# Performance work log

Measured on AMD Instinct MI355X. Metric: run time of the kernel, lower is better.

## Reference

```python
import jax, jax.numpy as jnp
import numpy as np

B, S, D, H, F, E, K = 2, 2048, 1024, 16, 4096, 8, 2
EPS = 1e-6


def setup_inputs() -> dict:
    key = jax.random.key(0)
    ks = jax.random.split(key, 9)
    s = 0.02
    return {
        "x": jax.random.normal(ks[0], (B, S, D), jnp.float32),
        "n1_w": jnp.ones((D,), jnp.float32),
        "n2_w": jnp.ones((D,), jnp.float32),
        "wq": jax.random.normal(ks[1], (D, D), jnp.float32) * s,
        "wk": jax.random.normal(ks[2], (D, D), jnp.float32) * s,
        "wv": jax.random.normal(ks[3], (D, D), jnp.float32) * s,
        "wo": jax.random.normal(ks[4], (D, D), jnp.float32) * s,
        "router_w": jax.random.normal(ks[5], (E, D), jnp.float32) * s,  # nn.Linear(D, E, bias=False)
        "w1": jax.random.normal(ks[6], (E, D, F), jnp.float32) * s,
        "b1": jnp.zeros((E, F), jnp.float32),
        "w2": jax.random.normal(ks[7], (E, F, D), jnp.float32) * s,
        "b2": jnp.zeros((E, D), jnp.float32),
    }


def _rms(t, w):
    return t * w * jax.lax.rsqrt(jnp.mean(t * t, axis=-1, keepdims=True) + EPS)


def reference(x, n1_w, n2_w, wq, wk, wv, wo, router_w, w1, b1, w2, b2):
    hd = D // H
    # --- pre-norm causal multi-head self-attention ---
    h = _rms(x, n1_w)
    q = (h @ wq).reshape(B, S, H, hd)
    k = (h @ wk).reshape(B, S, H, hd)
    v = (h @ wv).reshape(B, S, H, hd)
    scores = jnp.einsum("bqhd,bkhd->bhqk", q, k) * (hd ** -0.5)
    causal = jnp.tril(jnp.ones((S, S), bool))
    scores = jnp.where(causal, scores, jnp.float32(-1e9))
    attn = jax.nn.softmax(scores, axis=-1)
    attn_out = jnp.einsum("bhqk,bkhd->bqhd", attn, v).reshape(B, S, D) @ wo
    x = x + attn_out
    # --- pre-norm MoE MLP: dense experts + top-k weighted combine ---
    h2 = _rms(x, n2_w)
    logits = h2 @ router_w.T                         # [B,S,E]
    probs = jax.nn.softmax(logits, axis=-1)
    topv, topi = jax.lax.top_k(probs, K)             # [B,S,K]
    topv = topv / jnp.sum(topv, axis=-1, keepdims=True)  # renormalized top-k gates
    bi = jnp.arange(B)[:, None, None]
    si = jnp.arange(S)[None, :, None]
    gates = jnp.zeros_like(probs).at[bi, si, topi].set(topv)  # sparse gates [B,S,E]
    eh = jax.nn.gelu(jnp.einsum("bsd,edf->ebsf", h2, w1) + b1[:, None, None, :])
    eo = jnp.einsum("ebsf,efd->ebsd", eh, w2) + b2[:, None, None, :]
    y = jnp.einsum("ebsd,bse->bsd", eo, gates)
    return x + y
```

## Files before the change

### kernel.cpp

```cpp
#include <hip/hip_runtime.h>
#include <hip/hip_bf16.h>


typedef float fx4 __attribute__((ext_vector_type(4)));
typedef short sx4 __attribute__((ext_vector_type(4)));
typedef short sx8 __attribute__((ext_vector_type(8)));
typedef int ix2 __attribute__((ext_vector_type(2)));
typedef int ix4 __attribute__((ext_vector_type(4)));

#define DEVFN static __device__ __forceinline__
#define MFMA16(a, b, c) __builtin_amdgcn_mfma_f32_16x16x32_bf16((a), (b), (c), 0, 0, 0)

typedef __attribute__((address_space(1))) const void GASV;
typedef __attribute__((address_space(3))) void LASV;

DEVFN short f2bf(float f) {
  unsigned u = __float_as_uint(f);
  return (short)((u + 0x7FFFu + ((u >> 16) & 1u)) >> 16);
}
DEVFN float bf2f(short s) { return __uint_as_float(((unsigned)(unsigned short)s) << 16); }

DEVFN int cvt_pk_bf16(float a, float b) {
  int r;
  asm("v_cvt_pk_bf16_f32 %0, %1, %2" : "=v"(r) : "v"(a), "v"(b));
  return r;
}

DEVFN void gll16(const short* g, short* l) {
  __builtin_amdgcn_global_load_lds((GASV*)g, (LASV*)l, 16, 0, 0);
}

template <int BK>
DEVFN int swzr(int row) {
  if constexpr (BK == 64)
    return row & 7;
  else
    return (row ^ (row >> 2)) & 3;
}

DEVFN float fast_gelu(float x) {
  float u = 0.7978845608028654f * (x + 0.044715f * x * x * x);
  float e = __expf(2.0f * u);
  float t = 1.0f - 2.0f / (1.0f + e);
  return 0.5f * x * (1.0f + t);
}

DEVFN float wsum64(float v) {
#pragma unroll
  for (int m = 1; m < 64; m <<= 1) v += __shfl_xor(v, m);
  return v;
}

template <int SPLIT>
__global__ __launch_bounds__(256) void transpose_k(const float* in, short* oh, short* ol,
                                                   int R, int C) {
  __shared__ float t[64][65];
  const int c0 = blockIdx.x * 64, r0 = blockIdx.y * 64;
  const long long bofs = (long long)blockIdx.z * R * C;
  in += bofs;
  oh += bofs;
  if (SPLIT) ol += bofs;
  const int tid = threadIdx.x;
  const int rr = tid >> 4, cc4 = (tid & 15) * 4;
#pragma unroll
  for (int i = 0; i < 4; ++i) {
    int r = i * 16 + rr;
    fx4 v = *(const fx4*)(in + (long long)(r0 + r) * C + c0 + cc4);
    t[r][cc4] = v.x;
    t[r][cc4 + 1] = v.y;
    t[r][cc4 + 2] = v.z;
    t[r][cc4 + 3] = v.w;
  }
  __syncthreads();
#pragma unroll
  for (int i = 0; i < 4; ++i) {
    int oc = i * 16 + rr;
    sx4 hv, lv;
#pragma unroll
    for (int j = 0; j < 4; ++j) {
      float v = t[cc4 + j][oc];
      short hi = f2bf(v);
      hv[j] = hi;
      if (SPLIT) lv[j] = f2bf(v - bf2f(hi));
    }
    *(sx4*)(oh + (long long)(c0 + oc) * R + r0 + cc4) = hv;
    if (SPLIT) *(sx4*)(ol + (long long)(c0 + oc) * R + r0 + cc4) = lv;
  }
}

template <int SPLIT>
__global__ __launch_bounds__(256) void rms_k(const float* x, const float* w, short* hh,
                                             short* hl) {
  const int row = blockIdx.x, tid = threadIdx.x;
  const fx4 v = ((const fx4*)(x + (long long)row * 1024))[tid];
  float ss = v.x * v.x + v.y * v.y + v.z * v.z + v.w * v.w;
  ss = wsum64(ss);
  __shared__ float red[4];
  if ((tid & 63) == 0) red[tid >> 6] = ss;
  __syncthreads();
  ss = red[0] + red[1] + red[2] + red[3];
  const float rr = rsqrtf(ss * (1.0f / 1024.0f) + 1e-6f);
  const fx4 wv = ((const fx4*)w)[tid];
  float vals[4] = {v.x * wv.x * rr, v.y * wv.y * rr, v.z * wv.z * rr, v.w * wv.w * rr};
  sx4 oh, ol;
#pragma unroll
  for (int c = 0; c < 4; ++c) {
    short hi = f2bf(vals[c]);
    oh[c] = hi;
    if (SPLIT) ol[c] = f2bf(vals[c] - bf2f(hi));
  }
  ((sx4*)(hh + (long long)row * 1024))[tid] = oh;
  if (SPLIT) ((sx4*)(hl + (long long)row * 1024))[tid] = ol;
}

struct GemmArgs {
  const short *Ah, *Al, *Bh, *Bl;
  int K, lda, ldb, ldc;
  long long strideBe;
  short *out_h, *out_l;
  float* out_f;
  const float* bias;
  const int* tile_info;
  const float* row_gate;
  const int* row_token;
};

template <int TERMS, int BM, int BK, int BN, int EPI, int PIPE, int NTHR, int WCN>
__global__ __launch_bounds__(NTHR) void gemm_k(GemmArgs a) {
  const int tid = threadIdx.x, lane = tid & 63, wave = tid >> 6;
  const int gx = gridDim.x;
  const int nwg = gx * (int)gridDim.y;
  int flat = (int)blockIdx.y * gx + (int)blockIdx.x;
  flat = (flat & 7) * (nwg >> 3) + (flat >> 3);
  const int bx = flat % gx;
  const int by = flat / gx;

  int row0, expert = 0, valid = BM;
  if constexpr (EPI == 3 || EPI == 5) {
    const int* ti = a.tile_info + by * 4;
    expert = ti[0];
    row0 = ti[1];
    valid = ti[2];
    if (valid == 0) return;
  } else {
    row0 = by * BM;
  }
  const short* Ap = a.Ah;
  const short* Bp = a.Bh + ((EPI == 3 || EPI == 5) ? (long long)expert * a.strideBe : 0ll);
  const int kbeg = blockIdx.z * a.K;

  constexpr int CH = BK / 8;
  constexpr int NIA = (BM * CH) / NTHR;
  constexpr int NIB = (BN * CH) / NTHR;
  constexpr int ASZ = BM * BK;
  constexpr int BSZ = BN * BK;
  constexpr int WRN = (NTHR / 64) / WCN;
  constexpr int MI = BM / WRN / 16;
  constexpr int TN = BN / WCN / 16;
  constexpr int NB = PIPE ? 2 : 1;

  __shared__ short Ash[NB][ASZ];
  __shared__ short Bsh[NB][BSZ];
  __shared__ short Asl[TERMS == 3 ? NB : 1][TERMS == 3 ? ASZ : 1];
  __shared__ short Bsl[TERMS == 3 ? NB : 1][TERMS == 3 ? BSZ : 1];

  fx4 acc[MI][TN] = {};
  const int wr = wave / WCN, wc = wave % WCN;

  long long aoff[NIA];
#pragma unroll
  for (int i = 0; i < NIA; ++i) {
    int row = (i * NTHR + tid) / CH;
    if constexpr (EPI == 3)
      aoff[i] = (long long)a.row_token[row0 + row] * a.lda;
    else
      aoff[i] = (long long)(row0 + row) * a.lda;
  }

  auto stage = [&](int s, int k0) {
#pragma unroll
    for (int i = 0; i < NIA; ++i) {
      int t = i * NTHR + tid;
      int row = t / CH, c = t % CH;
      int cc = c ^ swzr<BK>(row);
      int lbase = (i * NTHR + wave * 64) * 8;
      long long acol = kbeg + k0 + cc * 8;
      gll16(Ap + aoff[i] + acol, &Ash[s][lbase]);
      if constexpr (TERMS == 3)
        gll16(a.Al + aoff[i] + acol, &Asl[s][lbase]);
    }
#pragma unroll
    for (int i = 0; i < NIB; ++i) {
      int t = i * NTHR + tid;
      int row = t / CH, c = t % CH;
      int cc = c ^ swzr<BK>(row);
      int lbase = (i * NTHR + wave * 64) * 8;
      long long acol = kbeg + k0 + cc * 8;
      gll16(Bp + (long long)(bx * BN + row) * a.ldb + acol, &Bsh[s][lbase]);
      if constexpr (TERMS == 3)
        gll16(a.Bl + (long long)(bx * BN + row) * a.ldb + acol, &Bsl[s][lbase]);
    }
  };

  auto compute = [&](int s) {
#pragma unroll
    for (int kk = 0; kk < BK / 32; ++kk) {
      sx8 ah[MI], bh[TN], al_[MI], bl_[TN];
#pragma unroll
      for (int mi = 0; mi < MI; ++mi) {
        int row = wr * (BM / WRN) + mi * 16 + (lane & 15);
        int sc = (kk * 4 + (lane >> 4)) ^ swzr<BK>(row);
        ah[mi] = *(const sx8*)&Ash[s][row * BK + sc * 8];
        if constexpr (TERMS == 3) al_[mi] = *(const sx8*)&Asl[s][row * BK + sc * 8];
      }
#pragma unroll
      for (int ni = 0; ni < TN; ++ni) {
        int row = wc * (BN / WCN) + ni * 16 + (lane & 15);
        int sc = (kk * 4 + (lane >> 4)) ^ swzr<BK>(row);
        bh[ni] = *(const sx8*)&Bsh[s][row * BK + sc * 8];
        if constexpr (TERMS == 3) bl_[ni] = *(const sx8*)&Bsl[s][row * BK + sc * 8];
      }
#pragma unroll
      for (int mi = 0; mi < MI; ++mi)
#pragma unroll
        for (int ni = 0; ni < TN; ++ni) {
          acc[mi][ni] = MFMA16(ah[mi], bh[ni], acc[mi][ni]);
          if constexpr (TERMS == 3) {
            acc[mi][ni] = MFMA16(ah[mi], bl_[ni], acc[mi][ni]);
            acc[mi][ni] = MFMA16(al_[mi], bh[ni], acc[mi][ni]);
          }
        }
    }
  };

  const int NT = a.K / BK;
  stage(0, 0);
  __syncthreads();
  for (int t = 0; t < NT; ++t) {
    if constexpr (PIPE) {
      if (t + 1 < NT) stage((t + 1) & 1, (t + 1) * BK);
      compute(t & 1);
      if (t + 1 < NT) __syncthreads();
    } else {
      compute(0);
      if (t + 1 < NT) {
        __syncthreads();
        stage(0, (t + 1) * BK);
        __syncthreads();
      }
    }
  }

#pragma unroll
  for (int mi = 0; mi < MI; ++mi)
#pragma unroll
    for (int ni = 0; ni < TN; ++ni) {
      fx4 v = acc[mi][ni];
      int rl = wr * (BM / WRN) + mi * 16 + ((lane >> 4) << 2);
      int col = bx * BN + wc * (BN / WCN) + ni * 16 + (lane & 15);
#pragma unroll
      for (int j = 0; j < 4; ++j) {
        int r = rl + j;
        long long grow = (long long)row0 + r;
        float xv = v[j];
        if constexpr (EPI == 1) {
          short hi = f2bf(xv);
          a.out_h[grow * a.ldc + col] = hi;
          a.out_l[grow * a.ldc + col] = f2bf(xv - bf2f(hi));
        } else if constexpr (EPI == 3) {
          xv += a.bias[expert * a.ldc + col];
          a.out_h[grow * a.ldc + col] = f2bf(fast_gelu(xv));
        } else if constexpr (EPI == 5) {
          if (r < valid) {
            xv += a.bias[expert * a.ldc + col];
            float g = a.row_gate[grow];
            a.out_h[grow * a.ldc + col] = f2bf(xv * g);
          }
        } else if constexpr (EPI == 6) {
          a.out_f[(long long)blockIdx.z * 4194304 + grow * a.ldc + col] = xv;
        }
      }
    }
}

__global__ __launch_bounds__(256) void combine_rms_router_k(
    const float* p0, const float* p1, const float* resid, const float* w,
    const float* rw, float* out, short* h2, int* tok_e, float* tok_g) {
  const int row = blockIdx.x, tid = threadIdx.x;
  const long long base = (long long)row * 1024 + tid * 4;
  fx4 a = *(const fx4*)(p0 + base);
  fx4 b = *(const fx4*)(p1 + base);
  fx4 r = *(const fx4*)(resid + base);
  fx4 o;
  float ss = 0.f;
#pragma unroll
  for (int j = 0; j < 4; ++j) {
    o[j] = a[j] + b[j] + r[j];
    ss += o[j] * o[j];
  }
  *(fx4*)(out + base) = o;
  ss = wsum64(ss);
  __shared__ float red[4];
  if ((tid & 63) == 0) red[tid >> 6] = ss;
  __syncthreads();
  ss = red[0] + red[1] + red[2] + red[3];
  const float rr = rsqrtf(ss * (1.0f / 1024.0f) + 1e-6f);
  const fx4 wv = ((const fx4*)w)[tid];
  fx4 t;
#pragma unroll
  for (int j = 0; j < 4; ++j) t[j] = o[j] * wv[j];
  sx4 oh;
#pragma unroll
  for (int c = 0; c < 4; ++c) oh[c] = f2bf(t[c] * rr);
  ((sx4*)(h2 + (long long)row * 1024))[tid] = oh;

  float lg[8];
#pragma unroll
  for (int e = 0; e < 8; ++e) {
    fx4 rv = ((const fx4*)(rw + e * 1024))[tid];
    float acc = t[0] * rv[0] + t[1] * rv[1] + t[2] * rv[2] + t[3] * rv[3];
    lg[e] = wsum64(acc);
  }
  __shared__ float lred[8][4];
  if ((tid & 63) == 0) {
#pragma unroll
    for (int e = 0; e < 8; ++e) lred[e][tid >> 6] = lg[e];
  }
  __syncthreads();
  if (tid == 0) {
    float logit[8];
#pragma unroll
    for (int e = 0; e < 8; ++e)
      logit[e] = (lred[e][0] + lred[e][1] + lred[e][2] + lred[e][3]) * rr;
    float mx = logit[0];
#pragma unroll
    for (int e = 1; e < 8; ++e) mx = fmaxf(mx, logit[e]);
    float pe[8];
#pragma unroll
    for (int e = 0; e < 8; ++e) pe[e] = expf(logit[e] - mx);
    int e1 = 0;
    float b1v = pe[0];
#pragma unroll
    for (int e = 1; e < 8; ++e)
      if (pe[e] > b1v) {
        b1v = pe[e];
        e1 = e;
      }
    int e2 = -1;
    float b2v = -1.0f;
#pragma unroll
    for (int e = 0; e < 8; ++e)
      if (e != e1 && pe[e] > b2v) {
        b2v = pe[e];
        e2 = e;
      }
    float inv = 1.0f / (b1v + b2v);
    tok_e[(long long)row * 2] = e1;
    tok_e[(long long)row * 2 + 1] = e2;
    tok_g[(long long)row * 2] = b1v * inv;
    tok_g[(long long)row * 2 + 1] = b2v * inv;
  }
}

__global__ __launch_bounds__(256) void combine_k(const int* row_of_entry,
                                                 const short* eo, float* out) {
  const int tid = threadIdx.x, lane = tid & 63, wave = tid >> 6;
  const long long token = (long long)blockIdx.x * 4 + wave;
  const int r1 = row_of_entry[token * 2];
  const int r2 = row_of_entry[token * 2 + 1];
  const sx8* e1 = (const sx8*)(eo + (long long)r1 * 1024);
  const sx8* e2 = (const sx8*)(eo + (long long)r2 * 1024);
  float* op = out + token * 1024;
#pragma unroll
  for (int half = 0; half < 2; ++half) {
    sx8 va = e1[lane + half * 64];
    sx8 vb = e2[lane + half * 64];
    int cb = (lane + half * 64) * 8;
#pragma unroll
    for (int q = 0; q < 2; ++q) {
      fx4 o = *(const fx4*)(op + cb + q * 4);
#pragma unroll
      for (int j = 0; j < 4; ++j) o[j] += bf2f(va[q * 4 + j]) + bf2f(vb[q * 4 + j]);
      *(fx4*)(op + cb + q * 4) = o;
    }
  }
}

__global__ __launch_bounds__(128, 2) void flash_k(const short* __restrict__ qkv_h,
                                                  const short* __restrict__ qkv_l,
                                                  short* __restrict__ ao_h,
                                                  short* __restrict__ ao_l) {
  const int tid = threadIdx.x, lane = tid & 63, wave = tid >> 6;
  const int l15 = lane & 15, g = lane >> 4;
  const int qt = (blockIdx.x + blockIdx.y) & 31;
  const int bh = blockIdx.y;
  const int b = bh >> 4, h = bh & 15;
  const long long base = (long long)b * 2048 * 3072;
  const int qw = qt * 64 + wave * 32;

  __shared__ short Kh[4096], Kl[4096];
  __shared__ int VTh[64 * 34], VTl[64 * 34];

  sx8 qh[2][2], ql[2][2];
#pragma unroll
  for (int mb = 0; mb < 2; ++mb)
#pragma unroll
    for (int kk = 0; kk < 2; ++kk) {
      long long qofs =
          base + (long long)(qw + mb * 16 + l15) * 3072 + h * 64 + kk * 32 + g * 8;
      qh[mb][kk] = *(const sx8*)(qkv_h + qofs);
      ql[mb][kk] = *(const sx8*)(qkv_l + qofs);
    }

  fx4 o[2][4] = {};
  float m_r[2] = {-3e38f, -3e38f}, l_r[2] = {0.f, 0.f};

  const int krow0 = tid >> 3;
  const int kc8 = (tid & 7) * 8;
  const int kswz = ((tid & 7) ^ (krow0 & 7)) * 8;
  const int vu = tid >> 3;
  const int vd0 = (tid & 7) * 8;

  sx8 kr[4], krl[4], vr[4], vrl[4];

  auto load_tile = [&](int kt2) {
    const long long tb = base + (long long)(kt2 * 64) * 3072 + h * 64;
#pragma unroll
    for (int s = 0; s < 4; ++s) {
      long long gofs = tb + 1024 + (long long)(s * 16 + krow0) * 3072 + kc8;
      kr[s] = *(const sx8*)(qkv_h + gofs);
      krl[s] = *(const sx8*)(qkv_l + gofs);
    }
#pragma unroll
    for (int k4 = 0; k4 < 4; ++k4) {
      long long gofs = tb + 2048 + (long long)(4 * vu + k4) * 3072 + vd0;
      vr[k4] = *(const sx8*)(qkv_h + gofs);
      vrl[k4] = *(const sx8*)(qkv_l + gofs);
    }
  };

  const int nt = qt + 1;
  load_tile(0);

  for (int kt = 0; kt < nt; ++kt) {
#pragma unroll
    for (int s = 0; s < 4; ++s) {
      *(sx8*)&Kh[(s * 16 + krow0) * 64 + kswz] = kr[s];
      *(sx8*)&Kl[(s * 16 + krow0) * 64 + kswz] = krl[s];
    }
#pragma unroll
    for (int i = 0; i < 8; ++i) {
      int d = vd0 + i;
      ix2 wh, wl;
      wh[0] = (int)(unsigned short)vr[0][i] | ((int)(unsigned short)vr[1][i] << 16);
      wh[1] = (int)(unsigned short)vr[2][i] | ((int)(unsigned short)vr[3][i] << 16);
      wl[0] = (int)(unsigned short)vrl[0][i] | ((int)(unsigned short)vrl[1][i] << 16);
      wl[1] = (int)(unsigned short)vrl[2][i] | ((int)(unsigned short)vrl[3][i] << 16);
      *(ix2*)&VTh[d * 34 + 2 * vu] = wh;
      *(ix2*)&VTl[d * 34 + 2 * vu] = wl;
    }
    __syncthreads();

    if (kt + 1 < nt) load_tile(kt + 1);

    const bool diag = (kt == nt - 1);
    float pvv[2][16];
#pragma unroll
    for (int kc = 0; kc < 4; ++kc) {
      int row = kc * 16 + l15;
      int rsw = row & 7;
      fx4 s0 = {}, s1 = {};
#pragma unroll
      for (int kk = 0; kk < 2; ++kk) {
        int sc = ((kk * 4 + g) ^ rsw) * 8;
        sx8 khf = *(const sx8*)&Kh[row * 64 + sc];
        sx8 klf = *(const sx8*)&Kl[row * 64 + sc];
        s0 = MFMA16(khf, qh[0][kk], s0);
        s1 = MFMA16(khf, qh[1][kk], s1);
        s0 = MFMA16(khf, ql[0][kk], s0);
        s1 = MFMA16(khf, ql[1][kk], s1);
        s0 = MFMA16(klf, qh[0][kk], s0);
        s1 = MFMA16(klf, qh[1][kk], s1);
      }
#pragma unroll
      for (int j = 0; j < 4; ++j) {
        pvv[0][kc * 4 + j] = s0[j];
        pvv[1][kc * 4 + j] = s1[j];
      }
    }

    sx8 pah[2][2], pal[2][2];
#pragma unroll
    for (int mb = 0; mb < 2; ++mb) {
      const int qidx = qw + mb * 16 + l15;
      float t[16];
      float tmax = -3e38f;
#pragma unroll
      for (int i = 0; i < 16; ++i) {
        float sv = pvv[mb][i] * 0.18033688011112f;
        if (diag) {
          int key = kt * 64 + (i >> 2) * 16 + g * 4 + (i & 3);
          sv = (key > qidx) ? -3e38f : sv;
        }
        t[i] = sv;
        tmax = fmaxf(tmax, sv);
      }
      tmax = fmaxf(tmax, __shfl_xor(tmax, 16));
      tmax = fmaxf(tmax, __shfl_xor(tmax, 32));
      if (__any(tmax > m_r[mb] + 8.0f)) {
        float mnew = fmaxf(m_r[mb], tmax);
        float al = exp2f(m_r[mb] - mnew);
        l_r[mb] *= al;
        float aj[4];
#pragma unroll
        for (int j = 0; j < 4; ++j) aj[j] = __shfl(al, (lane & 48) | (g << 2) | j);
#pragma unroll
        for (int f = 0; f < 4; ++f)
#pragma unroll
          for (int j = 0; j < 4; ++j) o[mb][f][j] *= aj[j];
        m_r[mb] = mnew;
      }
      float ps = 0.f;
#pragma unroll
      for (int i = 0; i < 16; ++i) {
        float e = exp2f(t[i] - m_r[mb]);
        t[i] = e;
        ps += e;
      }
      l_r[mb] += ps;
#pragma unroll
      for (int grp = 0; grp < 2; ++grp) {
        ix4 ih, il;
#pragma unroll
        for (int q2 = 0; q2 < 4; ++q2) {
          float a = t[grp * 8 + 2 * q2], bb = t[grp * 8 + 2 * q2 + 1];
          int I = cvt_pk_bf16(a, bb);
          float h0 = __uint_as_float((unsigned)I << 16);
          float h1 = __uint_as_float((unsigned)I & 0xffff0000u);
          int L = cvt_pk_bf16(a - h0, bb - h1);
          ih[q2] = I;
          il[q2] = L;
        }
        pah[mb][grp] = __builtin_bit_cast(sx8, ih);
        pal[mb][grp] = __builtin_bit_cast(sx8, il);
      }
    }

    const ix2* vth = (const ix2*)VTh;
    const ix2* vtl = (const ix2*)VTl;
#pragma unroll
    for (int f = 0; f < 4; ++f) {
      int dd = f * 16 + l15;
      ix2 a0 = vth[dd * 17 + g], a1 = vth[dd * 17 + 4 + g];
      ix2 a2 = vth[dd * 17 + 8 + g], a3 = vth[dd * 17 + 12 + g];
      ix2 c0 = vtl[dd * 17 + g], c1 = vtl[dd * 17 + 4 + g];
      ix2 c2 = vtl[dd * 17 + 8 + g], c3 = vtl[dd * 17 + 12 + g];
      ix4 w;
      w[0] = a0[0]; w[1] = a0[1]; w[2] = a1[0]; w[3] = a1[1];
      sx8 vh8a = __builtin_bit_cast(sx8, w);
      w[0] = a2[0]; w[1] = a2[1]; w[2] = a3[0]; w[3] = a3[1];
      sx8 vh8b = __builtin_bit_cast(sx8, w);
      w[0] = c0[0]; w[1] = c0[1]; w[2] = c1[0]; w[3] = c1[1];
      sx8 vl8a = __builtin_bit_cast(sx8, w);
      w[0] = c2[0]; w[1] = c2[1]; w[2] = c3[0]; w[3] = c3[1];
      sx8 vl8b = __builtin_bit_cast(sx8, w);
#pragma unroll
      for (int mb = 0; mb < 2; ++mb) {
        o[mb][f] = MFMA16(pah[mb][0], vh8a, o[mb][f]);
        o[mb][f] = MFMA16(pah[mb][0], vl8a, o[mb][f]);
        o[mb][f] = MFMA16(pal[mb][0], vh8a, o[mb][f]);
        o[mb][f] = MFMA16(pah[mb][1], vh8b, o[mb][f]);
        o[mb][f] = MFMA16(pah[mb][1], vl8b, o[mb][f]);
        o[mb][f] = MFMA16(pal[mb][1], vh8b, o[mb][f]);
      }
    }
    __syncthreads();
  }

#pragma unroll
  for (int mb = 0; mb < 2; ++mb) {
    float lt = l_r[mb];
    lt += __shfl_xor(lt, 16);
    lt += __shfl_xor(lt, 32);
    float linv = 1.0f / lt;
    float lj[4];
#pragma unroll
    for (int j = 0; j < 4; ++j) lj[j] = __shfl(linv, (lane & 48) | (g << 2) | j);
#pragma unroll
    for (int f = 0; f < 4; ++f)
#pragma unroll
      for (int j = 0; j < 4; ++j) {
        float val = o[mb][f][j] * lj[j];
        long long orow = (long long)b * 2048 + qw + mb * 16 + g * 4 + j;
        int ocol = h * 64 + f * 16 + l15;
        short hi = f2bf(val);
        ao_h[orow * 1024 + ocol] = hi;
        ao_l[orow * 1024 + ocol] = f2bf(val - bf2f(hi));
      }
  }
}

__global__ __launch_bounds__(1024) void rank_k(const int* tok_e, const float* tok_g,
                                               int* tinfo, int* row_of_entry,
                                               int* row_token, float* row_gate) {
  const int tid = threadIdx.x, lane = tid & 63, wave = tid >> 6;
  __shared__ unsigned wtot[16][4];
  __shared__ unsigned woff[16][4];
  __shared__ int segsh[8];
#pragma unroll
  for (int i = 0; i < 9; ++i) {
    int r = tid * 9 + i;
    if (r < 9216) {
      row_token[r] = 0;
      row_gate[r] = 0.f;
    }
  }
  int e[8];
  {
    const int4* te = (const int4*)tok_e;
    int4 a = te[tid * 2], b = te[tid * 2 + 1];
    e[0] = a.x; e[1] = a.y; e[2] = a.z; e[3] = a.w;
    e[4] = b.x; e[5] = b.y; e[6] = b.z; e[7] = b.w;
  }
  unsigned c0 = 0, c1 = 0, c2 = 0, c3 = 0;
#pragma unroll
  for (int i = 0; i < 8; ++i) {
    unsigned f = 1u << ((e[i] & 1) << 4);
    int h = e[i] >> 1;
    c0 += (h == 0) ? f : 0u;
    c1 += (h == 1) ? f : 0u;
    c2 += (h == 2) ? f : 0u;
    c3 += (h == 3) ? f : 0u;
  }
  unsigned s0 = c0, s1 = c1, s2 = c2, s3 = c3;
#pragma unroll
  for (int d = 1; d < 64; d <<= 1) {
    unsigned t0 = __shfl_up(s0, d), t1 = __shfl_up(s1, d);
    unsigned t2 = __shfl_up(s2, d), t3 = __shfl_up(s3, d);
    if (lane >= d) { s0 += t0; s1 += t1; s2 += t2; s3 += t3; }
  }
  if (lane == 63) {
    wtot[wave][0] = s0; wtot[wave][1] = s1; wtot[wave][2] = s2; wtot[wave][3] = s3;
  }
  __syncthreads();
  if (wave == 0 && lane < 16) {
    unsigned v0 = wtot[lane][0], v1 = wtot[lane][1];
    unsigned v2 = wtot[lane][2], v3 = wtot[lane][3];
    unsigned i0 = v0, i1 = v1, i2 = v2, i3 = v3;
#pragma unroll
    for (int d = 1; d < 16; d <<= 1) {
      unsigned t0 = __shfl_up(i0, d), t1 = __shfl_up(i1, d);
      unsigned t2 = __shfl_up(i2, d), t3 = __shfl_up(i3, d);
      if (lane >= d) { i0 += t0; i1 += t1; i2 += t2; i3 += t3; }
    }
    woff[lane][0] = i0 - v0; woff[lane][1] = i1 - v1;
    woff[lane][2] = i2 - v2; woff[lane][3] = i3 - v3;
    if (lane == 15) {
      wtot[0][0] = i0; wtot[0][1] = i1; wtot[0][2] = i2; wtot[0][3] = i3;
    }
  }
  __syncthreads();
  if (tid == 0) {
    int cnt[8], tte[8], total = 0;
    for (int ee = 0; ee < 8; ++ee) {
      unsigned tot = wtot[0][ee >> 1];
      cnt[ee] = (int)((tot >> ((ee & 1) * 16)) & 0xFFFFu);
      tte[ee] = (cnt[ee] + 127) >> 7;
      total += tte[ee];
    }
    for (int s2 = 0; s2 < 80; ++s2) tinfo[s2 * 4 + 2] = 0;
    int off = 0, i = 0;
    for (int ee = 0; ee < 8; ++ee) {
      segsh[ee] = off;
      for (int t2 = 0; t2 < tte[ee]; ++t2) {
        int slot = (i * 80) / total;
        tinfo[slot * 4 + 0] = ee;
        tinfo[slot * 4 + 1] = off + t2 * 128;
        int v = cnt[ee] - t2 * 128;
        tinfo[slot * 4 + 2] = v > 128 ? 128 : v;
        ++i;
      }
      off += tte[ee] << 7;
    }
  }
  __syncthreads();
  unsigned x0 = woff[wave][0] + s0 - c0;
  unsigned x1 = woff[wave][1] + s1 - c1;
  unsigned x2 = woff[wave][2] + s2 - c2;
  unsigned x3 = woff[wave][3] + s3 - c3;
  const int entry0 = tid * 8;
#pragma unroll
  for (int i = 0; i < 8; ++i) {
    int ee = e[i];
    int h = ee >> 1, sh = (ee & 1) << 4;
    unsigned px = (h == 0) ? x0 : (h == 1) ? x1 : (h == 2) ? x2 : x3;
    int rank = (int)((px >> sh) & 0xFFFFu);
    unsigned f = 1u << sh;
    x0 += (h == 0) ? f : 0u;
    x1 += (h == 1) ? f : 0u;
    x2 += (h == 2) ? f : 0u;
    x3 += (h == 3) ? f : 0u;
    int row = segsh[ee] + rank;
    row_of_entry[entry0 + i] = row;
    row_token[row] = (entry0 + i) >> 1;
    row_gate[row] = tok_g[entry0 + i];
  }
}

extern "C" void kernel_launch(void* const* d_in, const int* in_sizes, int n_in,
                              void* d_out, int out_size, void* d_ws, size_t ws_size,
                              hipStream_t stream) {
  (void)in_sizes;
  (void)n_in;
  (void)out_size;
  (void)ws_size;
  const float* x = (const float*)d_in[0];
  const float* n1w = (const float*)d_in[1];
  const float* n2w = (const float*)d_in[2];
  const float* wq = (const float*)d_in[3];
  const float* wk = (const float*)d_in[4];
  const float* wv = (const float*)d_in[5];
  const float* wo = (const float*)d_in[6];
  const float* rw = (const float*)d_in[7];
  const float* w1 = (const float*)d_in[8];
  const float* b1 = (const float*)d_in[9];
  const float* w2 = (const float*)d_in[10];
  const float* b2 = (const float*)d_in[11];
  float* out = (float*)d_out;
  char* ws = (char*)d_ws;

  short* wqkv_h = (short*)(ws + 0);
  short* wqkv_l = (short*)(ws + 6291456);
  short* wo_h = (short*)(ws + 12582912);
  short* wo_l = (short*)(ws + 14680064);
  short* h_h = (short*)(ws + 16777216);
  short* h_l = (short*)(ws + 25165824);
  short* qkv_h = (short*)(ws + 33554432);
  short* qkv_l = (short*)(ws + 58720256);
  short* ao_h = (short*)(ws + 83886080);
  short* ao_l = (short*)(ws + 92274688);
  float* wo_part = (float*)(ws + 100663296);
  short* h2 = (short*)(ws + 0);
  short* eo = (short*)(ws + 8388608);
  short* wslot = (short*)(ws + 27262976);
  int* row_of_entry = (int*)(ws + 94371840);
  short* eh = (short*)(ws + 100663296);
  char* ctrl = ws + 176160768;
  int* tinfo = (int*)(ctrl + 128);
  int* tok_e = (int*)(ctrl + 2048);
  float* tok_g = (float*)(ctrl + 2048 + 32768);
  int* row_token = (int*)(ctrl + 2048 + 65536);
  float* row_gate = (float*)(ctrl + 2048 + 65536 + 36864);

  transpose_k<1><<<dim3(16, 16, 1), 256, 0, stream>>>(wq, wqkv_h, wqkv_l, 1024, 1024);
  transpose_k<1><<<dim3(16, 16, 1), 256, 0, stream>>>(wk, wqkv_h + 1024 * 1024,
                                                      wqkv_l + 1024 * 1024, 1024, 1024);
  transpose_k<1><<<dim3(16, 16, 1), 256, 0, stream>>>(wv, wqkv_h + 2048 * 1024,
                                                      wqkv_l + 2048 * 1024, 1024, 1024);
  transpose_k<1><<<dim3(16, 16, 1), 256, 0, stream>>>(wo, wo_h, wo_l, 1024, 1024);

  rms_k<1><<<4096, 256, 0, stream>>>(x, n1w, h_h, h_l);

  {
    GemmArgs a = {};
    a.Ah = h_h;
    a.Al = h_l;
    a.Bh = wqkv_h;
    a.Bl = wqkv_l;
    a.K = 1024;
    a.lda = 1024;
    a.ldb = 1024;
    a.ldc = 3072;
    a.out_h = qkv_h;
    a.out_l = qkv_l;
    gemm_k<3, 128, 32, 128, 1, 1, 512, 4><<<dim3(24, 32), 512, 0, stream>>>(a);
  }

  flash_k<<<dim3(32, 32), 128, 0, stream>>>(qkv_h, qkv_l, ao_h, ao_l);

  {
    GemmArgs a = {};
    a.Ah = ao_h;
    a.Al = ao_l;
    a.Bh = wo_h;
    a.Bl = wo_l;
    a.K = 512;
    a.lda = 1024;
    a.ldb = 1024;
    a.ldc = 1024;
    a.out_f = wo_part;
    gemm_k<3, 128, 32, 128, 6, 1, 512, 4><<<dim3(8, 32, 2), 512, 0, stream>>>(a);
  }
  combine_rms_router_k<<<4096, 256, 0, stream>>>(wo_part, wo_part + 4194304, x, n2w,
                                                 rw, out, h2, tok_e, tok_g);

  rank_k<<<1, 1024, 0, stream>>>(tok_e, tok_g, tinfo, row_of_entry, row_token,
                                 row_gate);

  transpose_k<0><<<dim3(64, 16, 8), 256, 0, stream>>>(w1, wslot, nullptr, 1024, 4096);
  {
    GemmArgs a = {};
    a.Ah = h2;
    a.Bh = wslot;
    a.K = 1024;
    a.lda = 1024;
    a.ldb = 1024;
    a.ldc = 4096;
    a.strideBe = (long long)4096 * 1024;
    a.out_h = eh;
    a.bias = b1;
    a.tile_info = tinfo;
    a.row_token = row_token;
    gemm_k<1, 128, 32, 128, 3, 1, 512, 4><<<dim3(32, 80), 512, 0, stream>>>(a);
  }

  transpose_k<0><<<dim3(16, 64, 8), 256, 0, stream>>>(w2, wslot, nullptr, 4096, 1024);
  {
    GemmArgs a = {};
    a.Ah = eh;
    a.Bh = wslot;
    a.K = 4096;
    a.lda = 4096;
    a.ldb = 4096;
    a.ldc = 1024;
    a.strideBe = (long long)1024 * 4096;
    a.out_h = eo;
    a.bias = b2;
    a.tile_info = tinfo;
    a.row_gate = row_gate;
    gemm_k<1, 128, 32, 128, 5, 1, 512, 4><<<dim3(8, 80), 512, 0, stream>>>(a);
  }

  combine_k<<<1024, 256, 0, stream>>>(row_of_entry, eo, out);
}
```

Baseline: 615.0 us.

## Split long causal attention query tiles across two blocks with merge kernel

Query tiles 16-31 in the flash attention kernel are now split into two key-range halves processed by separate blocks. Each half writes unnormalized partial outputs plus its row max and row sum, and a new merge kernel combines them with log-sum-exp rescaling. This evens out per-block work in the causal triangle, reducing the tail from the longest blocks. The cost is an extra launch, a round trip of fp32 partials through global memory, and reuse of workspace that is shared with wo_part.

```diff
diff --git a/kernel.cpp b/kernel.cpp
--- a/kernel.cpp
+++ b/kernel.cpp
@@ -386,16 +386,30 @@
   }
 }
 
-__global__ __launch_bounds__(128, 2) void flash_k(const short* __restrict__ qkv_h,
-                                                  const short* __restrict__ qkv_l,
-                                                  short* __restrict__ ao_h,
-                                                  short* __restrict__ ao_l) {
+__global__ __launch_bounds__(128, 2) void flash_k(
+    const short* __restrict__ qkv_h, const short* __restrict__ qkv_l,
+    short* __restrict__ ao_h, short* __restrict__ ao_l, float* __restrict__ opart,
+    float* __restrict__ mpart, float* __restrict__ lpart) {
   const int tid = threadIdx.x, lane = tid & 63, wave = tid >> 6;
   const int l15 = lane & 15, g = lane >> 4;
-  const int qt = (blockIdx.x + blockIdx.y) & 31;
+  const int unit = ((int)blockIdx.x + (int)blockIdx.y) % 48;
   const int bh = blockIdx.y;
   const int b = bh >> 4, h = bh & 15;
   const long long base = (long long)b * 2048 * 3072;
+
+  int qt, kt0, kt1, halfp;
+  if (unit < 16) {
+    qt = unit;
+    kt0 = 0;
+    kt1 = qt + 1;
+    halfp = -1;
+  } else {
+    int idx = unit - 16;
+    qt = 16 + (idx >> 1);
+    halfp = idx & 1;
+    kt0 = halfp ? 16 : 0;
+    kt1 = halfp ? (qt + 1) : 16;
+  }
   const int qw = qt * 64 + wave * 32;
 
   __shared__ short Kh[4096], Kl[4096];
@@ -439,10 +453,9 @@
     }
   };
 
-  const int nt = qt + 1;
-  load_tile(0);
-
-  for (int kt = 0; kt < nt; ++kt) {
+  load_tile(kt0);
+
+  for (int kt = kt0; kt < kt1; ++kt) {
 #pragma unroll
     for (int s = 0; s < 4; ++s) {
       *(sx8*)&Kh[(s * 16 + krow0) * 64 + kswz] = kr[s];
@@ -461,9 +474,9 @@
     }
     __syncthreads();
 
-    if (kt + 1 < nt) load_tile(kt + 1);
-
-    const bool diag = (kt == nt - 1);
+    if (kt + 1 < kt1) load_tile(kt + 1);
+
+    const bool diag = (kt == qt);
     float pvv[2][16];
 #pragma unroll
     for (int kc = 0; kc < 4; ++kc) {
@@ -577,26 +590,93 @@
     __syncthreads();
   }
 
-#pragma unroll
-  for (int mb = 0; mb < 2; ++mb) {
-    float lt = l_r[mb];
-    lt += __shfl_xor(lt, 16);
-    lt += __shfl_xor(lt, 32);
-    float linv = 1.0f / lt;
-    float lj[4];
-#pragma unroll
-    for (int j = 0; j < 4; ++j) lj[j] = __shfl(linv, (lane & 48) | (g << 2) | j);
-#pragma unroll
-    for (int f = 0; f < 4; ++f)
+  if (halfp < 0) {
+#pragma unroll
+    for (int mb = 0; mb < 2; ++mb) {
+      float lt = l_r[mb];
+      lt += __shfl_xor(lt, 16);
+      lt += __shfl_xor(lt, 32);
+      float linv = 1.0f / lt;
+      float lj[4];
+#pragma unroll
+      for (int j = 0; j < 4; ++j) lj[j] = __shfl(linv, (lane & 48) | (g << 2) | j);
+#pragma unroll
+      for (int f = 0; f < 4; ++f)
+#pragma unroll
+        for (int j = 0; j < 4; ++j) {
+          float val = o[mb][f][j] * lj[j];
+          long long orow = (long long)b * 2048 + qw + mb * 16 + g * 4 + j;
+          int ocol = h * 64 + f * 16 + l15;
+          short hi = f2bf(val);
+          ao_h[orow * 1024 + ocol] = hi;
+          ao_l[orow * 1024 + ocol] = f2bf(val - bf2f(hi));
+        }
+    }
+  } else {
+    const int qti = qt - 16;
+    const long long pb = (long long)(halfp * 16 + qti) * 32 + bh;
+    float* op = opart + pb * 4096;
+#pragma unroll
+    for (int mb = 0; mb < 2; ++mb) {
+      float lt = l_r[mb];
+      lt += __shfl_xor(lt, 16);
+      lt += __shfl_xor(lt, 32);
+      float mj[4], ljv[4];
 #pragma unroll
       for (int j = 0; j < 4; ++j) {
-        float val = o[mb][f][j] * lj[j];
-        long long orow = (long long)b * 2048 + qw + mb * 16 + g * 4 + j;
-        int ocol = h * 64 + f * 16 + l15;
-        short hi = f2bf(val);
-        ao_h[orow * 1024 + ocol] = hi;
-        ao_l[orow * 1024 + ocol] = f2bf(val - bf2f(hi));
-      }
+        int src = (lane & 48) | (g << 2) | j;
+        mj[j] = __shfl(m_r[mb], src);
+        ljv[j] = __shfl(lt, src);
+      }
+#pragma unroll
+      for (int f = 0; f < 4; ++f)
+#pragma unroll
+        for (int j = 0; j < 4; ++j) {
+          int r = wave * 32 + mb * 16 + g * 4 + j;
+          int d = f * 16 + l15;
+          op[r * 64 + d] = o[mb][f][j];
+        }
+      if (l15 == 0) {
+#pragma unroll
+        for (int j = 0; j < 4; ++j) {
+          int r = wave * 32 + mb * 16 + g * 4 + j;
+          mpart[pb * 64 + r] = mj[j];
+          lpart[pb * 64 + r] = ljv[j];
+        }
+      }
+    }
+  }
+}
+
+__global__ __launch_bounds__(256) void merge_k(const float* opart, const float* mpart,
+                                               const float* lpart, short* ao_h,
+                                               short* ao_l) {
+  const int qti = blockIdx.x, bh = blockIdx.y;
+  const int b = bh >> 4, h = bh & 15;
+  const int tid = threadIdx.x;
+  const int r = tid >> 2, d0 = (tid & 3) * 16;
+  const long long pb0 = (long long)qti * 32 + bh;
+  const long long pb1 = (long long)(16 + qti) * 32 + bh;
+  const float m1 = mpart[pb0 * 64 + r], m2 = mpart[pb1 * 64 + r];
+  const float l1 = lpart[pb0 * 64 + r], l2 = lpart[pb1 * 64 + r];
+  const float M = fmaxf(m1, m2);
+  const float w1 = exp2f(m1 - M), w2 = exp2f(m2 - M);
+  const float inv = 1.0f / (l1 * w1 + l2 * w2);
+  const float* o1 = opart + pb0 * 4096 + r * 64 + d0;
+  const float* o2 = opart + pb1 * 4096 + r * 64 + d0;
+  const long long orow = (long long)b * 2048 + (16 + qti) * 64 + r;
+  const int ocol = h * 64 + d0;
+#pragma unroll
+  for (int q = 0; q < 4; ++q) {
+    fx4 a = *(const fx4*)(o1 + q * 4);
+    fx4 c = *(const fx4*)(o2 + q * 4);
+#pragma unroll
+    for (int j = 0; j < 4; ++j) {
+      float val = (a[j] * w1 + c[j] * w2) * inv;
+      short hi = f2bf(val);
+      ao_h[orow * 1024 + ocol + q * 4 + j] = hi;
+      ao_l[orow * 1024 + ocol + q * 4 + j] = f2bf(val - bf2f(hi));
+    }
   }
 }
 
@@ -739,6 +819,9 @@
   short* qkv_l = (short*)(ws + 58720256);
   short* ao_h = (short*)(ws + 83886080);
   short* ao_l = (short*)(ws + 92274688);
+  float* opart = (float*)(ws + 100663296);
+  float* mpart = (float*)(ws + 117440512);
+  float* lpart = (float*)(ws + 117702656);
   float* wo_part = (float*)(ws + 100663296);
   short* h2 = (short*)(ws + 0);
   short* eo = (short*)(ws + 8388608);
@@ -776,7 +859,9 @@
     gemm_k<3, 128, 32, 128, 1, 1, 512, 4><<<dim3(24, 32), 512, 0, stream>>>(a);
   }
 
-  flash_k<<<dim3(32, 32), 128, 0, stream>>>(qkv_h, qkv_l, ao_h, ao_l);
+  flash_k<<<dim3(48, 32), 128, 0, stream>>>(qkv_h, qkv_l, ao_h, ao_l, opart, mpart,
+                                            lpart);
+  merge_k<<<dim3(16, 32), 256, 0, stream>>>(opart, mpart, lpart, ao_h, ao_l);
 
   {
     GemmArgs a = {};
```

New measurement: 627.7 us. 1.02x slower.

## Split flash attention query tile across four waves of 16 rows each

Applied to the files above, without the earlier changes.

The flash attention kernel now uses 256 threads (4 waves) per 64-query block, each wave owning 16 query rows instead of 32. Per-thread register state (Q fragments, O accumulators, softmax stats, staged K/V tiles) is halved, and the cooperative K/V tile load and V transpose are spread over twice as many threads. The aim is more waves in flight to hide latency. In exchange, each wave reuses every K/V LDS read for fewer MFMAs and more waves contend at the barriers.

```diff
diff --git a/kernel.cpp b/kernel.cpp
--- a/kernel.cpp
+++ b/kernel.cpp
@@ -386,7 +386,7 @@
   }
 }
 
-__global__ __launch_bounds__(128, 2) void flash_k(const short* __restrict__ qkv_h,
+__global__ __launch_bounds__(256, 2) void flash_k(const short* __restrict__ qkv_h,
                                                   const short* __restrict__ qkv_l,
                                                   short* __restrict__ ao_h,
                                                   short* __restrict__ ao_l) {
@@ -396,24 +396,21 @@
   const int bh = blockIdx.y;
   const int b = bh >> 4, h = bh & 15;
   const long long base = (long long)b * 2048 * 3072;
-  const int qw = qt * 64 + wave * 32;
+  const int qw = qt * 64 + wave * 16;
 
   __shared__ short Kh[4096], Kl[4096];
   __shared__ int VTh[64 * 34], VTl[64 * 34];
 
-  sx8 qh[2][2], ql[2][2];
-#pragma unroll
-  for (int mb = 0; mb < 2; ++mb)
-#pragma unroll
-    for (int kk = 0; kk < 2; ++kk) {
-      long long qofs =
-          base + (long long)(qw + mb * 16 + l15) * 3072 + h * 64 + kk * 32 + g * 8;
-      qh[mb][kk] = *(const sx8*)(qkv_h + qofs);
-      ql[mb][kk] = *(const sx8*)(qkv_l + qofs);
-    }
-
-  fx4 o[2][4] = {};
-  float m_r[2] = {-3e38f, -3e38f}, l_r[2] = {0.f, 0.f};
+  sx8 qh[2], ql[2];
+#pragma unroll
+  for (int kk = 0; kk < 2; ++kk) {
+    long long qofs = base + (long long)(qw + l15) * 3072 + h * 64 + kk * 32 + g * 8;
+    qh[kk] = *(const sx8*)(qkv_h + qofs);
+    ql[kk] = *(const sx8*)(qkv_l + qofs);
+  }
+
+  fx4 o[4] = {};
+  float m_r = -3e38f, l_r = 0.f;
 
   const int krow0 = tid >> 3;
   const int kc8 = (tid & 7) * 8;
@@ -421,19 +418,19 @@
   const int vu = tid >> 3;
   const int vd0 = (tid & 7) * 8;
 
-  sx8 kr[4], krl[4], vr[4], vrl[4];
+  sx8 kr[2], krl[2], vr[2], vrl[2];
 
   auto load_tile = [&](int kt2) {
     const long long tb = base + (long long)(kt2 * 64) * 3072 + h * 64;
 #pragma unroll
-    for (int s = 0; s < 4; ++s) {
-      long long gofs = tb + 1024 + (long long)(s * 16 + krow0) * 3072 + kc8;
+    for (int s = 0; s < 2; ++s) {
+      long long gofs = tb + 1024 + (long long)(s * 32 + krow0) * 3072 + kc8;
       kr[s] = *(const sx8*)(qkv_h + gofs);
       krl[s] = *(const sx8*)(qkv_l + gofs);
     }
 #pragma unroll
-    for (int k4 = 0; k4 < 4; ++k4) {
-      long long gofs = tb + 2048 + (long long)(4 * vu + k4) * 3072 + vd0;
+    for (int k4 = 0; k4 < 2; ++k4) {
+      long long gofs = tb + 2048 + (long long)(2 * vu + k4) * 3072 + vd0;
       vr[k4] = *(const sx8*)(qkv_h + gofs);
       vrl[k4] = *(const sx8*)(qkv_l + gofs);
     }
@@ -444,60 +441,50 @@
 
   for (int kt = 0; kt < nt; ++kt) {
 #pragma unroll
-    for (int s = 0; s < 4; ++s) {
-      *(sx8*)&Kh[(s * 16 + krow0) * 64 + kswz] = kr[s];
-      *(sx8*)&Kl[(s * 16 + krow0) * 64 + kswz] = krl[s];
+    for (int s = 0; s < 2; ++s) {
+      *(sx8*)&Kh[(s * 32 + krow0) * 64 + kswz] = kr[s];
+      *(sx8*)&Kl[(s * 32 + krow0) * 64 + kswz] = krl[s];
     }
 #pragma unroll
     for (int i = 0; i < 8; ++i) {
       int d = vd0 + i;
-      ix2 wh, wl;
-      wh[0] = (int)(unsigned short)vr[0][i] | ((int)(unsigned short)vr[1][i] << 16);
-      wh[1] = (int)(unsigned short)vr[2][i] | ((int)(unsigned short)vr[3][i] << 16);
-      wl[0] = (int)(unsigned short)vrl[0][i] | ((int)(unsigned short)vrl[1][i] << 16);
-      wl[1] = (int)(unsigned short)vrl[2][i] | ((int)(unsigned short)vrl[3][i] << 16);
-      *(ix2*)&VTh[d * 34 + 2 * vu] = wh;
-      *(ix2*)&VTl[d * 34 + 2 * vu] = wl;
+      int wh = (int)(unsigned short)vr[0][i] | ((int)(unsigned short)vr[1][i] << 16);
+      int wl = (int)(unsigned short)vrl[0][i] | ((int)(unsigned short)vrl[1][i] << 16);
+      VTh[d * 34 + vu] = wh;
+      VTl[d * 34 + vu] = wl;
     }
     __syncthreads();
 
     if (kt + 1 < nt) load_tile(kt + 1);
 
     const bool diag = (kt == nt - 1);
-    float pvv[2][16];
+    float pvv[16];
 #pragma unroll
     for (int kc = 0; kc < 4; ++kc) {
       int row = kc * 16 + l15;
       int rsw = row & 7;
-      fx4 s0 = {}, s1 = {};
+      fx4 s0 = {};
 #pragma unroll
       for (int kk = 0; kk < 2; ++kk) {
         int sc = ((kk * 4 + g) ^ rsw) * 8;
         sx8 khf = *(const sx8*)&Kh[row * 64 + sc];
         sx8 klf = *(const sx8*)&Kl[row * 64 + sc];
-        s0 = MFMA16(khf, qh[0][kk], s0);
-        s1 = MFMA16(khf, qh[1][kk], s1);
-        s0 = MFMA16(khf, ql[0][kk], s0);
-        s1 = MFMA16(khf, ql[1][kk], s1);
-        s0 = MFMA16(klf, qh[0][kk], s0);
-        s1 = MFMA16(klf, qh[1][kk], s1);
-      }
-#pragma unroll
-      for (int j = 0; j < 4; ++j) {
-        pvv[0][kc * 4 + j] = s0[j];
-        pvv[1][kc * 4 + j] = s1[j];
-      }
-    }
-
-    sx8 pah[2][2], pal[2][2];
-#pragma unroll
-    for (int mb = 0; mb < 2; ++mb) {
-      const int qidx = qw + mb * 16 + l15;
+        s0 = MFMA16(khf, qh[kk], s0);
+        s0 = MFMA16(khf, ql[kk], s0);
+        s0 = MFMA16(klf, qh[kk], s0);
+      }
+#pragma unroll
+      for (int j = 0; j < 4; ++j) pvv[kc * 4 + j] = s0[j];
+    }
+
+    sx8 pah[2], pal[2];
+    {
+      const int qidx = qw + l15;
       float t[16];
       float tmax = -3e38f;
 #pragma unroll
       for (int i = 0; i < 16; ++i) {
-        float sv = pvv[mb][i] * 0.18033688011112f;
+        float sv = pvv[i] * 0.18033688011112f;
         if (diag) {
           int key = kt * 64 + (i >> 2) * 16 + g * 4 + (i & 3);
           sv = (key > qidx) ? -3e38f : sv;
@@ -507,27 +494,27 @@
       }
       tmax = fmaxf(tmax, __shfl_xor(tmax, 16));
       tmax = fmaxf(tmax, __shfl_xor(tmax, 32));
-      if (__any(tmax > m_r[mb] + 8.0f)) {
-        float mnew = fmaxf(m_r[mb], tmax);
-        float al = exp2f(m_r[mb] - mnew);
-        l_r[mb] *= al;
+      if (__any(tmax > m_r + 8.0f)) {
+        float mnew = fmaxf(m_r, tmax);
+        float al = exp2f(m_r - mnew);
+        l_r *= al;
         float aj[4];
 #pragma unroll
         for (int j = 0; j < 4; ++j) aj[j] = __shfl(al, (lane & 48) | (g << 2) | j);
 #pragma unroll
         for (int f = 0; f < 4; ++f)
 #pragma unroll
-          for (int j = 0; j < 4; ++j) o[mb][f][j] *= aj[j];
-        m_r[mb] = mnew;
+          for (int j = 0; j < 4; ++j) o[f][j] *= aj[j];
+        m_r = mnew;
       }
       float ps = 0.f;
 #pragma unroll
       for (int i = 0; i < 16; ++i) {
-        float e = exp2f(t[i] - m_r[mb]);
+        float e = exp2f(t[i] - m_r);
         t[i] = e;
         ps += e;
       }
-      l_r[mb] += ps;
+      l_r += ps;
 #pragma unroll
       for (int grp = 0; grp < 2; ++grp) {
         ix4 ih, il;
@@ -541,8 +528,8 @@
           ih[q2] = I;
           il[q2] = L;
         }
-        pah[mb][grp] = __builtin_bit_cast(sx8, ih);
-        pal[mb][grp] = __builtin_bit_cast(sx8, il);
+        pah[grp] = __builtin_bit_cast(sx8, ih);
+        pal[grp] = __builtin_bit_cast(sx8, il);
       }
     }
 
@@ -564,22 +551,18 @@
       sx8 vl8a = __builtin_bit_cast(sx8, w);
       w[0] = c2[0]; w[1] = c2[1]; w[2] = c3[0]; w[3] = c3[1];
       sx8 vl8b = __builtin_bit_cast(sx8, w);
-#pragma unroll
-      for (int mb = 0; mb < 2; ++mb) {
-        o[mb][f] = MFMA16(pah[mb][0], vh8a, o[mb][f]);
-        o[mb][f] = MFMA16(pah[mb][0], vl8a, o[mb][f]);
-        o[mb][f] = MFMA16(pal[mb][0], vh8a, o[mb][f]);
-        o[mb][f] = MFMA16(pah[mb][1], vh8b, o[mb][f]);
-        o[mb][f] = MFMA16(pah[mb][1], vl8b, o[mb][f]);
-        o[mb][f] = MFMA16(pal[mb][1], vh8b, o[mb][f]);
-      }
+      o[f] = MFMA16(pah[0], vh8a, o[f]);
+      o[f] = MFMA16(pah[0], vl8a, o[f]);
+      o[f] = MFMA16(pal[0], vh8a, o[f]);
+      o[f] = MFMA16(pah[1], vh8b, o[f]);
+      o[f] = MFMA16(pah[1], vl8b, o[f]);
+      o[f] = MFMA16(pal[1], vh8b, o[f]);
     }
     __syncthreads();
   }
 
-#pragma unroll
-  for (int mb = 0; mb < 2; ++mb) {
-    float lt = l_r[mb];
+  {
+    float lt = l_r;
     lt += __shfl_xor(lt, 16);
     lt += __shfl_xor(lt, 32);
     float linv = 1.0f / lt;
@@ -590,8 +573,8 @@
     for (int f = 0; f < 4; ++f)
 #pragma unroll
       for (int j = 0; j < 4; ++j) {
-        float val = o[mb][f][j] * lj[j];
-        long long orow = (long long)b * 2048 + qw + mb * 16 + g * 4 + j;
+        float val = o[f][j] * lj[j];
+        long long orow = (long long)b * 2048 + qw + g * 4 + j;
         int ocol = h * 64 + f * 16 + l15;
         short hi = f2bf(val);
         ao_h[orow * 1024 + ocol] = hi;
@@ -776,7 +759,7 @@
     gemm_k<3, 128, 32, 128, 1, 1, 512, 4><<<dim3(24, 32), 512, 0, stream>>>(a);
   }
 
-  flash_k<<<dim3(32, 32), 128, 0, stream>>>(qkv_h, qkv_l, ao_h, ao_l);
+  flash_k<<<dim3(32, 32), 256, 0, stream>>>(qkv_h, qkv_l, ao_h, ao_l);
 
   {
     GemmArgs a = {};
```

New measurement: 615.3 us. About the same (+0.0%).
